# Kernel tuning notes

Measured on AMD Instinct MI355X. Metric: run time of the kernel, lower is better.

Reference implementation:

```python
import jax, jax.numpy as jnp
import numpy as np

B, CIN, P = 256, 128, 27
DIM, NCLS, COUT = 512, 16, 128
FC1_IN = 128 * 5 * 5  # conv stack on 27x27: 25->12->10->5


def conv2d(x, w, b):
    # x: [B,C,H,W], w: [O,I,kh,kw] (torch OIHW layout), VALID padding, stride 1
    y = jax.lax.conv_general_dilated(x, w, (1, 1), 'VALID',
                                     dimension_numbers=('NCHW', 'OIHW', 'NCHW'))
    return y + b[None, :, None, None]


def maxpool2(x):
    return jax.lax.reduce_window(x, -jnp.inf, jax.lax.max,
                                 (1, 1, 2, 2), (1, 1, 2, 2), 'VALID')


def essa(x, w_qkv, b_qkv, w_ln, b_ln):
    Bs, C, H, W = x.shape
    N = H * W
    t = x.reshape(Bs, C, N).transpose(0, 2, 1)          # [B,N,C]
    qkv = t @ w_qkv + b_qkv                              # [B,N,3C]
    q, k, v = jnp.split(qkv, 3, axis=-1)
    q = q - q.mean(-1, keepdims=True)
    k = k - k.mean(-1, keepdims=True)
    q2 = q * q
    k2 = k * k
    q2 = q2 / (q2.sum(-1, keepdims=True) + 1e-7)
    k2 = k2 / (k2.sum(-1, keepdims=True) + 1e-7)
    # F.normalize: L2-normalize q2 over channel dim, k2 over token dim
    q2 = q2 / jnp.maximum(jnp.linalg.norm(q2, axis=-1, keepdims=True), 1e-12)
    k2 = k2 / jnp.maximum(jnp.linalg.norm(k2, axis=-2, keepdims=True), 1e-12)
    kv = jnp.einsum('bnc,bnd->bcd', k2, v)               # [B,C,C]
    t2 = jnp.einsum('bnc,bcd->bnd', q2, kv) / float(np.sqrt(N))
    attn = (v + t2) @ w_ln + b_ln                        # [B,N,C]
    return attn.transpose(0, 2, 1).reshape(Bs, C, H, W)


def setup_inputs() -> dict:
    key = jax.random.key(0)
    ks = jax.random.split(key, 20)
    s = 0.02
    d = {
        'x': jax.random.normal(ks[0], (B, CIN, P, P), jnp.float32),
        'w_qkv': jax.random.normal(ks[1], (CIN, 3 * CIN), jnp.float32) * s,
        'b_qkv': jnp.zeros((3 * CIN,), jnp.float32),
        'w_ln': jax.random.normal(ks[2], (CIN, CIN), jnp.float32) * s,
        'b_ln': jnp.zeros((CIN,), jnp.float32),
        'w_ffn1': jax.random.normal(ks[3], (64, 2 * CIN, 1, 1), jnp.float32) * s,
        'b_ffn1': jnp.zeros((64,), jnp.float32),
        'w_ffn2': jax.random.normal(ks[4], (CIN, 64, 1, 1), jnp.float32) * s,
        'b_ffn2': jnp.zeros((CIN,), jnp.float32),
        'w_c1': jax.random.normal(ks[5], (64, CIN, 3, 3), jnp.float32) * s,
        'b_c1': jnp.zeros((64,), jnp.float32),
        'w_c2': jax.random.normal(ks[6], (128, 64, 3, 3), jnp.float32) * s,
        'b_c2': jnp.zeros((128,), jnp.float32),
        'w_fc1': jax.random.normal(ks[7], (FC1_IN, DIM), jnp.float32) * s,
        'b_fc1': jnp.zeros((DIM,), jnp.float32),
        'w_fc2': jax.random.normal(ks[8], (DIM, DIM), jnp.float32) * s,
        'b_fc2': jnp.zeros((DIM,), jnp.float32),
        'w_cls': jax.random.normal(ks[9], (DIM, NCLS), jnp.float32) * s,
        'b_cls': jnp.zeros((NCLS,), jnp.float32),
    }
    return d


def reference(x, w_qkv, b_qkv, w_ln, b_ln, w_ffn1, b_ffn1, w_ffn2, b_ffn2,
              w_c1, b_c1, w_c2, b_c2, w_fc1, b_fc1, w_fc2, b_fc2, w_cls, b_cls):
    x_essa = essa(x, w_qkv, b_qkv, w_ln, b_ln)
    cat = jnp.concatenate([x, x_essa], axis=1)           # [B,2C,H,W]
    h = jax.nn.leaky_relu(conv2d(cat, w_ffn1, b_ffn1))   # slope 0.01 = torch default
    x_en = conv2d(h, w_ffn2, b_ffn2) + x
    o1 = maxpool2(jax.nn.relu(conv2d(x_en, w_c1, b_c1)))
    o2 = maxpool2(jax.nn.relu(conv2d(o1, w_c2, b_c2)))
    o2 = o2.reshape(o2.shape[0], -1)                     # [B,3200]
    o3 = jax.nn.relu(o2 @ w_fc1 + b_fc1)
    o4 = jax.nn.relu(o3 @ w_fc2 + b_fc2)
    return o4 @ w_cls + b_cls                            # [B,num_classes]
```

## Files before the change

### kernel.cpp

```cpp
#include <hip/hip_runtime.h>
#include <hip/hip_bf16.h>

#define HB 256
#define HC 128
#define HN 729
#define NP 732
#define NT2 736

typedef __attribute__((ext_vector_type(8))) short bf16x8;
typedef __attribute__((ext_vector_type(4))) float f32x4;
typedef __attribute__((ext_vector_type(4))) unsigned int uint4v;
typedef unsigned short u16;

#define MFMA16(a,b,c) __builtin_amdgcn_mfma_f32_16x16x32_bf16((a),(b),(c),0,0,0)

__device__ __forceinline__ float wsum(float v) {
    #pragma unroll
    for (int m = 32; m >= 1; m >>= 1) v += __shfl_xor(v, m, 64);
    return v;
}
__device__ __forceinline__ u16 f2b(float f) {
    __hip_bfloat16 h = __float2bfloat16(f);
    return *reinterpret_cast<u16*>(&h);
}
__device__ __forceinline__ float b2f(u16 u) {
    __hip_bfloat16 h;
    *reinterpret_cast<u16*>(&h) = u;
    return __bfloat162float(h);
}
__device__ __forceinline__ unsigned int pk2(u16 a, u16 b) {
    return (unsigned int)a | ((unsigned int)b << 16);
}

__device__ __forceinline__ void stage_tile(char* lds, const u16* src, long srcK,
                                           int row0, int rowLim, int k0, int kLim,
                                           int R, int tid)
{
    for (int t = tid; t < R*8; t += 256) {
        int r = t >> 3, s = t & 7;
        uint4v val = {0u,0u,0u,0u};
        int gr = row0 + r;
        if (gr < rowLim && (k0 + s*8) < kLim)
            val = *(const uint4v*)(src + (long)gr*srcK + k0 + s*8);
        *(uint4v*)(lds + r*128 + ((s ^ (r & 7)) << 4)) = val;
    }
}
__device__ __forceinline__ bf16x8 frag_ld(const char* lds, int rbase, int k0, int lane)
{
    int r = rbase + (lane & 15);
    int s = (k0 >> 3) + (lane >> 4);
    return *(const bf16x8*)(lds + r*128 + ((s ^ (r & 7)) << 4));
}

__global__ void k_prep(const float* __restrict__ wf1, const float* __restrict__ wf2,
                       const float* __restrict__ wc1, const float* __restrict__ wc2,
                       const float* __restrict__ wqkv, const float* __restrict__ wln,
                       float* __restrict__ w1t, float* __restrict__ w2t,
                       u16* __restrict__ wqkvT, u16* __restrict__ wlnT,
                       u16* __restrict__ w1b, u16* __restrict__ w2b)
{
    int idx = blockIdx.x*256 + threadIdx.x;
    if (idx < 73728) {
        int row = idx >> 6, oc = idx & 63;
        int ic = row/9, tap = row - ic*9;
        w1t[idx] = wc1[(oc*128 + ic)*9 + tap];
    } else if (idx < 147456) {
        int t = idx - 73728; int row = t >> 7, oc = t & 127;
        int ic = row/9, tap = row - ic*9;
        w2t[t] = wc2[(oc*64 + ic)*9 + tap];
    } else if (idx < 196608) {
        int t = idx - 147456; int o = t >> 7, k = t & 127;
        wqkvT[t] = f2b(wqkv[k*384 + o]);
    } else if (idx < 212992) {
        int t = idx - 196608; int o = t >> 7, k = t & 127;
        wlnT[t] = f2b(wln[k*128 + o]);
    } else if (idx < 229376) {
        int t = idx - 212992;
        w1b[t] = f2b(wf1[t]);
    } else if (idx < 237568) {
        int t = idx - 229376;
        w2b[t] = f2b(wf2[t]);
    }
}

__global__ __launch_bounds__(256) void k_xbt(const float* __restrict__ x, u16* __restrict__ xbt)
{
    __shared__ float T[64*129];
    const int b = blockIdx.y, n0 = blockIdx.x*64, tid = threadIdx.x;
    for (int idx = tid; idx < 128*64; idx += 256) {
        int c = idx >> 6, j = idx & 63;
        int n = n0 + j;
        T[j*129 + c] = (n < HN) ? x[(size_t)(b*128 + c)*HN + n] : 0.f;
    }
    __syncthreads();
    for (int idx = tid; idx < 64*16; idx += 256) {
        int m = idx >> 4, cs = idx & 15;
        int n = n0 + m;
        if (n < HN) {
            const float* p = &T[m*129 + cs*8];
            uint4v V = { pk2(f2b(p[0]), f2b(p[1])), pk2(f2b(p[2]), f2b(p[3])),
                         pk2(f2b(p[4]), f2b(p[5])), pk2(f2b(p[6]), f2b(p[7])) };
            *(uint4v*)(xbt + ((long)b*HN + n)*128 + cs*8) = V;
        }
    }
}

__global__ __launch_bounds__(256) void k_gqkv(
    const u16* __restrict__ xbt, const u16* __restrict__ wqkvT, const float* __restrict__ bqkv,
    u16* __restrict__ qb, u16* __restrict__ kb, u16* __restrict__ vbt)
{
    __shared__ __align__(16) char smem[8192 + 49152];
    char* As = smem;
    char* Bs = smem + 8192;
    const int b = blockIdx.y, n0 = blockIdx.x*64, tid = threadIdx.x;
    const int lane = tid & 63, w = tid >> 6;
    f32x4 acc[4][6];
    #pragma unroll
    for (int i = 0; i < 4; ++i)
        #pragma unroll
        for (int j = 0; j < 6; ++j) acc[i][j] = (f32x4){0.f,0.f,0.f,0.f};
    const u16* Ab = xbt + (long)b*HN*128;
    for (int kt = 0; kt < 128; kt += 64) {
        stage_tile(As, Ab, 128, n0, HN, kt, 128, 64, tid);
        stage_tile(Bs, wqkvT, 128, 0, 384, kt, 128, 384, tid);
        __syncthreads();
        #pragma unroll
        for (int k0 = 0; k0 < 64; k0 += 32) {
            bf16x8 bf[6];
            #pragma unroll
            for (int j = 0; j < 6; ++j) bf[j] = frag_ld(Bs, (w*6 + j)*16, k0, lane);
            #pragma unroll
            for (int m = 0; m < 4; ++m) {
                bf16x8 af = frag_ld(As, m*16, k0, lane);
                #pragma unroll
                for (int j = 0; j < 6; ++j) acc[m][j] = MFMA16(af, bf[j], acc[m][j]);
            }
        }
        __syncthreads();
    }
    u16* E = (u16*)Bs;
    #pragma unroll
    for (int m = 0; m < 4; ++m)
        #pragma unroll
        for (int j = 0; j < 6; ++j) {
            int col = w*96 + j*16 + (lane & 15);
            float bia = bqkv[col];
            #pragma unroll
            for (int i = 0; i < 4; ++i) {
                int row = m*16 + (lane >> 4)*4 + i;
                E[row*384 + col] = f2b(acc[m][j][i] + bia);
            }
        }
    __syncthreads();
    for (int t = tid; t < 64*48; t += 256) {
        int r = t / 48, cs = t - r*48;
        int n = n0 + r;
        if (n < HN) {
            int col = cs*8;
            u16* dst = (col < 128) ? qb : (col < 256) ? kb : vbt;
            *(uint4v*)(dst + ((long)b*HN + n)*128 + (col & 127)) = *(const uint4v*)(E + r*384 + col);
        }
    }
}

__global__ __launch_bounds__(256) void k_postq(u16* __restrict__ qb)
{
    const int b = blockIdx.y;
    const int n = blockIdx.x*4 + (threadIdx.x >> 6);
    const int lane = threadIdx.x & 63;
    if (n >= HN) return;
    u16* p = qb + ((long)b*HN + n)*128;
    unsigned int u = *(const unsigned int*)(p + 2*lane);
    float f0 = b2f((u16)(u & 0xffff));
    float f1 = b2f((u16)(u >> 16));
    float m = wsum(f0 + f1) * (1.f/128.f);
    float a0 = f0 - m, a1 = f1 - m;
    float s0 = a0*a0, s1 = a1*a1;
    float S  = wsum(s0 + s1);
    float s4 = wsum(s0*s0 + s1*s1);
    float invS = 1.f / (S + 1e-7f);
    float nrm = sqrtf(s4) * invS;
    float sc = invS / fmaxf(nrm, 1e-12f);
    *(unsigned int*)(p + 2*lane) = pk2(f2b(s0*sc), f2b(s1*sc));
}

__global__ __launch_bounds__(256) void k_postk(const u16* __restrict__ kb, u16* __restrict__ k2t)
{
    __shared__ u16 KT[64*130];
    const int b = blockIdx.y, n0 = blockIdx.x*64, tid = threadIdx.x;
    const int lane = tid & 63, w = tid >> 6;
    for (int it = 0; it < 16; ++it) {
        int r = w*16 + it;
        int n = n0 + r;
        float f0 = 0.f, f1 = 0.f;
        if (n < HN) {
            unsigned int u = *(const unsigned int*)(kb + ((long)b*HN + n)*128 + 2*lane);
            f0 = b2f((u16)(u & 0xffff));
            f1 = b2f((u16)(u >> 16));
        }
        float m = wsum(f0 + f1) * (1.f/128.f);
        float a0 = f0 - m, a1 = f1 - m;
        float s0 = a0*a0, s1 = a1*a1;
        float S = wsum(s0 + s1);
        float invS = 1.f/(S + 1e-7f);
        *(unsigned int*)&KT[r*130 + 2*lane] = pk2(f2b(s0*invS), f2b(s1*invS));
    }
    __syncthreads();
    #pragma unroll
    for (int pass = 0; pass < 4; ++pass) {
        int c = pass*32 + (tid >> 3), j8 = tid & 7;
        u16 v[8];
        #pragma unroll
        for (int j = 0; j < 8; ++j) {
            int r = j8*8 + j;
            v[j] = (n0 + r < HN) ? KT[r*130 + c] : (u16)0;
        }
        int n = n0 + j8*8;
        if (n < NT2) {
            uint4v V = { pk2(v[0],v[1]), pk2(v[2],v[3]), pk2(v[4],v[5]), pk2(v[6],v[7]) };
            *(uint4v*)(k2t + ((long)b*128 + c)*NT2 + n) = V;
        }
    }
}

__global__ __launch_bounds__(256) void k_vT(const u16* __restrict__ vbt, u16* __restrict__ vtt)
{
    __shared__ u16 T[64*130];
    const int b = blockIdx.y, n0 = blockIdx.x*64, tid = threadIdx.x;
    for (int t = tid; t < 64*16; t += 256) {
        int r = t >> 4, cs = t & 15;
        int n = n0 + r;
        uint4v val = {0u,0u,0u,0u};
        if (n < HN) val = *(const uint4v*)(vbt + ((long)b*HN + n)*128 + cs*8);
        #pragma unroll
        for (int e = 0; e < 4; ++e)
            *(unsigned int*)&T[r*130 + cs*8 + e*2] = val[e];
    }
    __syncthreads();
    #pragma unroll
    for (int pass = 0; pass < 4; ++pass) {
        int d = pass*32 + (tid >> 3), j8 = tid & 7;
        u16 v[8];
        #pragma unroll
        for (int j = 0; j < 8; ++j) {
            int r = j8*8 + j;
            v[j] = (n0 + r < HN) ? T[r*130 + d] : (u16)0;
        }
        int n = n0 + j8*8;
        if (n < NT2) {
            uint4v V = { pk2(v[0],v[1]), pk2(v[2],v[3]), pk2(v[4],v[5]), pk2(v[6],v[7]) };
            *(uint4v*)(vtt + ((long)b*128 + d)*NT2 + n) = V;
        }
    }
}

__global__ __launch_bounds__(256) void k_coln(const u16* __restrict__ k2t, float* __restrict__ cn)
{
    long row = (long)blockIdx.x*4 + (threadIdx.x >> 6);
    int lane = threadIdx.x & 63;
    const u16* p = k2t + row*NT2;
    float s = 0.f;
    for (int i = lane; i < NT2/2; i += 64) {
        unsigned int u = *(const unsigned int*)(p + 2*i);
        float f0 = b2f((u16)(u & 0xffff));
        float f1 = b2f((u16)(u >> 16));
        s += f0*f0 + f1*f1;
    }
    s = wsum(s);
    if (lane == 0) cn[row] = 1.f / fmaxf(sqrtf(s), 1e-12f);
}

__global__ __launch_bounds__(256) void k_gkv(
    const u16* __restrict__ vtt, const u16* __restrict__ k2t,
    const float* __restrict__ cn, u16* __restrict__ kvT)
{
    __shared__ __align__(16) char smem[8192 + 16384 + 512];
    char* As = smem;
    char* Bs = smem + 8192;
    float* CNs = (float*)(smem + 8192 + 16384);
    const int b = blockIdx.y, d0 = blockIdx.x*64, tid = threadIdx.x;
    const int lane = tid & 63, w = tid >> 6;
    if (tid < 128) CNs[tid] = cn[b*128 + tid];
    f32x4 acc[4][2];
    #pragma unroll
    for (int i = 0; i < 4; ++i) { acc[i][0] = (f32x4){0,0,0,0}; acc[i][1] = (f32x4){0,0,0,0}; }
    const u16* Ab = vtt + (long)b*128*NT2;
    const u16* Bb = k2t + (long)b*128*NT2;
    for (int kt = 0; kt < NT2; kt += 64) {
        stage_tile(As, Ab, NT2, d0, 128, kt, NT2, 64, tid);
        stage_tile(Bs, Bb, NT2, 0, 128, kt, NT2, 128, tid);
        __syncthreads();
        #pragma unroll
        for (int k0 = 0; k0 < 64; k0 += 32) {
            bf16x8 bf[2];
            bf[0] = frag_ld(Bs, (w*2 + 0)*16, k0, lane);
            bf[1] = frag_ld(Bs, (w*2 + 1)*16, k0, lane);
            #pragma unroll
            for (int m = 0; m < 4; ++m) {
                bf16x8 af = frag_ld(As, m*16, k0, lane);
                acc[m][0] = MFMA16(af, bf[0], acc[m][0]);
                acc[m][1] = MFMA16(af, bf[1], acc[m][1]);
            }
        }
        __syncthreads();
    }
    u16* E = (u16*)Bs;
    #pragma unroll
    for (int m = 0; m < 4; ++m)
        #pragma unroll
        for (int j = 0; j < 2; ++j) {
            int col = w*32 + j*16 + (lane & 15);
            float s = CNs[col];
            #pragma unroll
            for (int i = 0; i < 4; ++i) {
                int row = m*16 + (lane >> 4)*4 + i;
                E[row*128 + col] = f2b(acc[m][j][i] * s);
            }
        }
    __syncthreads();
    for (int t = tid; t < 64*16; t += 256) {
        int r = t >> 4, cs = t & 15;
        *(uint4v*)(kvT + ((long)b*128 + d0 + r)*128 + cs*8) = *(const uint4v*)(E + r*128 + cs*8);
    }
}

__global__ __launch_bounds__(256) void k_gt2u(
    const u16* __restrict__ q2b, const u16* __restrict__ kvT,
    const u16* __restrict__ vbt, u16* __restrict__ ubt)
{
    __shared__ __align__(16) char smem[8192 + 16384];
    char* As = smem;
    char* Bs = smem + 8192;
    const int b = blockIdx.y, n0 = blockIdx.x*64, tid = threadIdx.x;
    const int lane = tid & 63, w = tid >> 6;
    f32x4 acc[4][2];
    #pragma unroll
    for (int i = 0; i < 4; ++i) { acc[i][0] = (f32x4){0,0,0,0}; acc[i][1] = (f32x4){0,0,0,0}; }
    const u16* Ab = q2b + (long)b*HN*128;
    const u16* Bb = kvT + (long)b*128*128;
    for (int kt = 0; kt < 128; kt += 64) {
        stage_tile(As, Ab, 128, n0, HN, kt, 128, 64, tid);
        stage_tile(Bs, Bb, 128, 0, 128, kt, 128, 128, tid);
        __syncthreads();
        #pragma unroll
        for (int k0 = 0; k0 < 64; k0 += 32) {
            bf16x8 bf[2];
            bf[0] = frag_ld(Bs, (w*2 + 0)*16, k0, lane);
            bf[1] = frag_ld(Bs, (w*2 + 1)*16, k0, lane);
            #pragma unroll
            for (int m = 0; m < 4; ++m) {
                bf16x8 af = frag_ld(As, m*16, k0, lane);
                acc[m][0] = MFMA16(af, bf[0], acc[m][0]);
                acc[m][1] = MFMA16(af, bf[1], acc[m][1]);
            }
        }
        __syncthreads();
    }
    u16* E = (u16*)Bs;
    const float sc = 1.f/27.f;
    #pragma unroll
    for (int m = 0; m < 4; ++m)
        #pragma unroll
        for (int j = 0; j < 2; ++j) {
            int col = w*32 + j*16 + (lane & 15);
            #pragma unroll
            for (int i = 0; i < 4; ++i) {
                int row = m*16 + (lane >> 4)*4 + i;
                E[row*128 + col] = f2b(acc[m][j][i] * sc);
            }
        }
    __syncthreads();
    for (int t = tid; t < 64*16; t += 256) {
        int r = t >> 4, cs = t & 15;
        int n = n0 + r;
        if (n < HN) {
            const u16* ep = E + r*128 + cs*8;
            const u16* vp = vbt + ((long)b*HN + n)*128 + cs*8;
            unsigned int wds[4];
            #pragma unroll
            for (int e = 0; e < 4; ++e)
                wds[e] = pk2(f2b(b2f(ep[e*2]) + b2f(vp[e*2])),
                             f2b(b2f(ep[e*2+1]) + b2f(vp[e*2+1])));
            uint4v V = { wds[0], wds[1], wds[2], wds[3] };
            *(uint4v*)(ubt + ((long)b*HN + n)*128 + cs*8) = V;
        }
    }
}

__global__ __launch_bounds__(256) void k_gattn(
    const u16* __restrict__ ubt, const u16* __restrict__ wlnT, const float* __restrict__ bln,
    u16* __restrict__ attnb)
{
    __shared__ __align__(16) char smem[8192 + 16384 + 512];
    char* As = smem;
    char* Bs = smem + 8192;
    float* BIAS = (float*)(smem + 8192 + 16384);
    const int b = blockIdx.y, n0 = blockIdx.x*64, tid = threadIdx.x;
    const int lane = tid & 63, w = tid >> 6;
    if (tid < 128) BIAS[tid] = bln[tid];
    f32x4 acc[4][2];
    #pragma unroll
    for (int i = 0; i < 4; ++i) { acc[i][0] = (f32x4){0,0,0,0}; acc[i][1] = (f32x4){0,0,0,0}; }
    const u16* Ab = ubt + (long)b*HN*128;
    for (int kt = 0; kt < 128; kt += 64) {
        stage_tile(As, Ab, 128, n0, HN, kt, 128, 64, tid);
        stage_tile(Bs, wlnT, 128, 0, 128, kt, 128, 128, tid);
        __syncthreads();
        #pragma unroll
        for (int k0 = 0; k0 < 64; k0 += 32) {
            bf16x8 bf[2];
            bf[0] = frag_ld(Bs, (w*2 + 0)*16, k0, lane);
            bf[1] = frag_ld(Bs, (w*2 + 1)*16, k0, lane);
            #pragma unroll
            for (int m = 0; m < 4; ++m) {
                bf16x8 af = frag_ld(As, m*16, k0, lane);
                acc[m][0] = MFMA16(af, bf[0], acc[m][0]);
                acc[m][1] = MFMA16(af, bf[1], acc[m][1]);
            }
        }
        __syncthreads();
    }
    u16* E = (u16*)Bs;
    #pragma unroll
    for (int m = 0; m < 4; ++m)
        #pragma unroll
        for (int j = 0; j < 2; ++j) {
            int col = w*32 + j*16 + (lane & 15);
            float bia = BIAS[col];
            #pragma unroll
            for (int i = 0; i < 4; ++i) {
                int row = m*16 + (lane >> 4)*4 + i;
                E[row*128 + col] = f2b(acc[m][j][i] + bia);
            }
        }
    __syncthreads();
    for (int t = tid; t < 64*16; t += 256) {
        int r = t >> 4, cs = t & 15;
        int n = n0 + r;
        if (n < HN)
            *(uint4v*)(attnb + ((long)b*HN + n)*128 + cs*8) = *(const uint4v*)(E + r*128 + cs*8);
    }
}

__global__ __launch_bounds__(256) void k_gffn1(
    const u16* __restrict__ xbt, const u16* __restrict__ attnb,
    const u16* __restrict__ w1b, const float* __restrict__ b1,
    u16* __restrict__ hb)
{
    __shared__ __align__(16) char smem[8192 + 8192 + 256];
    char* As = smem;
    char* Bs = smem + 8192;
    float* BIAS = (float*)(smem + 16384);
    const int b = blockIdx.y, n0 = blockIdx.x*64, tid = threadIdx.x;
    const int lane = tid & 63, w = tid >> 6;
    if (tid < 64) BIAS[tid] = b1[tid];
    f32x4 acc[4];
    #pragma unroll
    for (int i = 0; i < 4; ++i) acc[i] = (f32x4){0,0,0,0};
    const u16* Ax = xbt + (long)b*HN*128;
    const u16* Aa = attnb + (long)b*HN*128;
    for (int kt = 0; kt < 256; kt += 64) {
        if (kt < 128) stage_tile(As, Ax, 128, n0, HN, kt, 128, 64, tid);
        else          stage_tile(As, Aa, 128, n0, HN, kt - 128, 128, 64, tid);
        stage_tile(Bs, w1b, 256, 0, 64, kt, 256, 64, tid);
        __syncthreads();
        #pragma unroll
        for (int k0 = 0; k0 < 64; k0 += 32) {
            bf16x8 bf = frag_ld(Bs, w*16, k0, lane);
            #pragma unroll
            for (int m = 0; m < 4; ++m) {
                bf16x8 af = frag_ld(As, m*16, k0, lane);
                acc[m] = MFMA16(af, bf, acc[m]);
            }
        }
        __syncthreads();
    }
    u16* E = (u16*)Bs;
    #pragma unroll
    for (int m = 0; m < 4; ++m) {
        int col = w*16 + (lane & 15);
        float bia = BIAS[col];
        #pragma unroll
        for (int i = 0; i < 4; ++i) {
            int row = m*16 + (lane >> 4)*4 + i;
            float v = acc[m][i] + bia;
            E[row*64 + col] = f2b((v > 0.f) ? v : 0.01f*v);
        }
    }
    __syncthreads();
    for (int t = tid; t < 64*8; t += 256) {
        int r = t >> 3, cs = t & 7;
        int n = n0 + r;
        if (n < HN)
            *(uint4v*)(hb + ((long)b*HN + n)*64 + cs*8) = *(const uint4v*)(E + r*64 + cs*8);
    }
}

__global__ __launch_bounds__(256) void k_gffn2(
    const u16* __restrict__ hb, const u16* __restrict__ w2b, const float* __restrict__ b2,
    const float* __restrict__ x, float* __restrict__ xen)
{
    __shared__ __align__(16) char smem[8192 + 16384 + 512];
    char* As = smem;
    char* Bs = smem + 8192;
    float* BIAS = (float*)(smem + 8192 + 16384);
    const int b = blockIdx.y, n0 = blockIdx.x*64, tid = threadIdx.x;
    const int lane = tid & 63, w = tid >> 6;
    if (tid < 128) BIAS[tid] = b2[tid];
    f32x4 acc[4][2];
    #pragma unroll
    for (int i = 0; i < 4; ++i) { acc[i][0] = (f32x4){0,0,0,0}; acc[i][1] = (f32x4){0,0,0,0}; }
    const u16* Ab = hb + (long)b*HN*64;
    stage_tile(As, Ab, 64, n0, HN, 0, 64, 64, tid);
    stage_tile(Bs, w2b, 64, 0, 128, 0, 64, 128, tid);
    __syncthreads();
    #pragma unroll
    for (int k0 = 0; k0 < 64; k0 += 32) {
        bf16x8 bf[2];
        bf[0] = frag_ld(Bs, (w*2 + 0)*16, k0, lane);
        bf[1] = frag_ld(Bs, (w*2 + 1)*16, k0, lane);
        #pragma unroll
        for (int m = 0; m < 4; ++m) {
            bf16x8 af = frag_ld(As, m*16, k0, lane);
            acc[m][0] = MFMA16(af, bf[0], acc[m][0]);
            acc[m][1] = MFMA16(af, bf[1], acc[m][1]);
        }
    }
    __syncthreads();
    u16* E = (u16*)Bs;
    #pragma unroll
    for (int m = 0; m < 4; ++m)
        #pragma unroll
        for (int j = 0; j < 2; ++j) {
            int col = w*32 + j*16 + (lane & 15);
            float bia = BIAS[col];
            #pragma unroll
            for (int i = 0; i < 4; ++i) {
                int row = m*16 + (lane >> 4)*4 + i;
                E[row*128 + col] = f2b(acc[m][j][i] + bia);
            }
        }
    __syncthreads();
    #pragma unroll
    for (int pass = 0; pass < 16; ++pass) {
        int c = pass*8 + (tid >> 5), jj = tid & 31;
        int r = jj*2;
        int n = n0 + r;
        const float* xrow = x + ((long)b*128 + c)*HN;
        float* orow = xen + ((long)b*128 + c)*NP;
        if (n + 1 < HN) {
            float x0 = xrow[n], x1 = xrow[n+1];
            float2 ov;
            ov.x = b2f(E[r*128 + c]) + x0;
            ov.y = b2f(E[(r+1)*128 + c]) + x1;
            *(float2*)(orow + n) = ov;
        } else if (n < HN) {
            orow[n] = b2f(E[r*128 + c]) + xrow[n];
        }
    }
}

__global__ __launch_bounds__(256) void k_conv1(
    const float* __restrict__ xen, const float* __restrict__ w1t, const float* __restrict__ bias,
    float* __restrict__ pool1)
{
    __shared__ __align__(16) float XT[16*280];
    __shared__ __align__(16) float W[144*64];
    const int b = blockIdx.y;
    const int ty = blockIdx.x * 8;
    const int tid = threadIdx.x;
    const int row = tid & 7, og = tid >> 3;
    float acc[24][2] = {};
    for (int ic0 = 0; ic0 < 128; ic0 += 16) {
        __syncthreads();
        for (int idx = tid; idx < 4480; idx += 256) {
            int icc = idx / 280; int rem = idx - icc*280;
            int iy = rem / 28, ix = rem - iy*28;
            XT[idx] = (ix < 27) ? xen[((size_t)b*128 + ic0 + icc)*NP + (ty+iy)*27 + ix] : 0.f;
        }
        for (int idx = tid; idx < 9216; idx += 256) W[idx] = w1t[ic0*9*64 + idx];
        __syncthreads();
        for (int icc = 0; icc < 16; ++icc) {
            #pragma unroll
            for (int dy = 0; dy < 3; ++dy) {
                const float* ar = &XT[icc*280 + (row+dy)*28];
                float a[28];
                #pragma unroll
                for (int t = 0; t < 7; ++t) {
                    float4 f = *(const float4*)&ar[t*4];
                    a[t*4]=f.x; a[t*4+1]=f.y; a[t*4+2]=f.z; a[t*4+3]=f.w;
                }
                #pragma unroll
                for (int dx = 0; dx < 3; ++dx) {
                    float2 wv = *(const float2*)&W[(icc*9 + dy*3 + dx)*64 + og*2];
                    #pragma unroll
                    for (int px = 0; px < 24; ++px) {
                        acc[px][0] += a[px+dx]*wv.x;
                        acc[px][1] += a[px+dx]*wv.y;
                    }
                }
            }
        }
    }
    float b0 = bias[og*2], b1 = bias[og*2+1];
    float m[12][2];
    #pragma unroll
    for (int p = 0; p < 12; ++p) {
        float p00 = fmaxf(acc[2*p][0]+b0, 0.f), p10 = fmaxf(acc[2*p+1][0]+b0, 0.f);
        float p01 = fmaxf(acc[2*p][1]+b1, 0.f), p11 = fmaxf(acc[2*p+1][1]+b1, 0.f);
        m[p][0] = fmaxf(p00,p10); m[p][1] = fmaxf(p01,p11);
    }
    #pragma unroll
    for (int p = 0; p < 12; ++p) {
        m[p][0] = fmaxf(m[p][0], __shfl_xor(m[p][0], 1, 64));
        m[p][1] = fmaxf(m[p][1], __shfl_xor(m[p][1], 1, 64));
    }
    if ((row & 1) == 0) {
        int py = (ty + row) >> 1;
        #pragma unroll
        for (int p = 0; p < 12; ++p)
            *(float2*)&pool1[(((size_t)b*12 + py)*12 + p)*64 + og*2] = make_float2(m[p][0], m[p][1]);
    }
}

__global__ __launch_bounds__(256) void k_conv2(
    const float* __restrict__ pool1, const float* __restrict__ w2t, const float* __restrict__ bias,
    float* __restrict__ pool2)
{
    __shared__ __align__(16) float XT[8*144];
    __shared__ __align__(16) float W[72*32];
    const int b = blockIdx.y;
    const int oc0 = blockIdx.x * 32;
    const int tid = threadIdx.x;
    const int row = tid & 15, og = tid >> 4;
    float acc[10][2] = {};
    for (int ic0 = 0; ic0 < 64; ic0 += 8) {
        __syncthreads();
        for (int idx = tid; idx < 8*144; idx += 256) {
            int icc = idx & 7, pix = idx >> 3;
            XT[icc*144 + pix] = pool1[((size_t)b*144 + pix)*64 + ic0 + icc];
        }
        for (int idx = tid; idx < 72*32; idx += 256) {
            int r = idx >> 5, o = idx & 31;
            W[idx] = w2t[(ic0*9 + r)*128 + oc0 + o];
        }
        __syncthreads();
        if (row < 10) {
            for (int icc = 0; icc < 8; ++icc) {
                #pragma unroll
                for (int dy = 0; dy < 3; ++dy) {
                    const float* ar = &XT[icc*144 + (row+dy)*12];
                    float a[12];
                    #pragma unroll
                    for (int t = 0; t < 3; ++t) {
                        float4 f = *(const float4*)&ar[t*4];
                        a[t*4]=f.x; a[t*4+1]=f.y; a[t*4+2]=f.z; a[t*4+3]=f.w;
                    }
                    #pragma unroll
                    for (int dx = 0; dx < 3; ++dx) {
                        float2 wv = *(const float2*)&W[(icc*9 + dy*3 + dx)*32 + og*2];
                        #pragma unroll
                        for (int px = 0; px < 10; ++px) {
                            acc[px][0] += a[px+dx]*wv.x;
                            acc[px][1] += a[px+dx]*wv.y;
                        }
                    }
                }
            }
        }
    }
    float b0 = bias[oc0+og*2], b1 = bias[oc0+og*2+1];
    float m[5][2] = {};
    if (row < 10) {
        #pragma unroll
        for (int p = 0; p < 5; ++p) {
            float p00 = fmaxf(acc[2*p][0]+b0, 0.f), p10 = fmaxf(acc[2*p+1][0]+b0, 0.f);
            float p01 = fmaxf(acc[2*p][1]+b1, 0.f), p11 = fmaxf(acc[2*p+1][1]+b1, 0.f);
            m[p][0] = fmaxf(p00,p10); m[p][1] = fmaxf(p01,p11);
        }
    }
    #pragma unroll
    for (int p = 0; p < 5; ++p) {
        m[p][0] = fmaxf(m[p][0], __shfl_xor(m[p][0], 1, 64));
        m[p][1] = fmaxf(m[p][1], __shfl_xor(m[p][1], 1, 64));
    }
    if (row < 10 && (row & 1) == 0) {
        int py = row >> 1;
        #pragma unroll
        for (int p = 0; p < 5; ++p)
            *(float2*)&pool2[(((size_t)b*5 + py)*5 + p)*128 + oc0 + og*2] = make_float2(m[p][0], m[p][1]);
    }
}

__global__ void k_permute(const float* __restrict__ pool2, float* __restrict__ o2t)
{
    int k = blockIdx.x;
    int b = threadIdx.x;
    int c = k / 25, r = k - c*25;
    o2t[(size_t)k*256 + b] = pool2[((size_t)b*25 + r)*128 + c];
}

__global__ __launch_bounds__(256) void k_fc1(
    const float* __restrict__ o2t, const float* __restrict__ wfc1, float* __restrict__ part)
{
    __shared__ __align__(16) float A[64*64];
    __shared__ __align__(16) float W[64*64];
    const int m0 = blockIdx.x*64, nn0 = blockIdx.y*64, s = blockIdx.z;
    const int tid = threadIdx.x, tq = tid & 15, og = tid >> 4;
    float acc[4][4] = {};
    for (int chunk = s; chunk < 50; chunk += 4) {
        int k0 = chunk*64;
        __syncthreads();
        for (int idx = tid; idx < 4096; idx += 256) {
            int kk = idx >> 6, mm = idx & 63;
            A[idx] = o2t[(size_t)(k0+kk)*256 + m0 + mm];
        }
        for (int idx = tid; idx < 4096; idx += 256) {
            int kk = idx >> 6, nn = idx & 63;
            W[idx] = wfc1[(size_t)(k0+kk)*512 + nn0 + nn];
        }
        __syncthreads();
        for (int kk = 0; kk < 64; ++kk) {
            float4 a = *(const float4*)&A[kk*64 + tq*4];
            float4 wv = *(const float4*)&W[kk*64 + og*4];
            float av[4] = {a.x,a.y,a.z,a.w};
            float wl[4] = {wv.x,wv.y,wv.z,wv.w};
            #pragma unroll
            for (int i = 0; i < 4; ++i)
                #pragma unroll
                for (int jj = 0; jj < 4; ++jj) acc[i][jj] += av[i]*wl[jj];
        }
    }
    #pragma unroll
    for (int jn = 0; jn < 4; ++jn) {
        int n = nn0 + og*4 + jn;
        float4 o4 = make_float4(acc[0][jn], acc[1][jn], acc[2][jn], acc[3][jn]);
        *(float4*)&part[((size_t)s*512 + n)*256 + m0 + tq*4] = o4;
    }
}

__global__ void k_fc1red(const float* __restrict__ part, const float* __restrict__ bias,
                         float* __restrict__ o3t)
{
    int idx = blockIdx.x*256 + threadIdx.x;
    int n = idx >> 8, m = idx & 255;
    float vs = bias[n];
    #pragma unroll
    for (int s = 0; s < 4; ++s) vs += part[((size_t)s*512 + n)*256 + m];
    o3t[idx] = fmaxf(vs, 0.f);
}

__global__ __launch_bounds__(256) void k_fc2(
    const float* __restrict__ o3t, const float* __restrict__ wfc2, const float* __restrict__ bias,
    float* __restrict__ o4t)
{
    __shared__ __align__(16) float A[64*64];
    __shared__ __align__(16) float W[64*64];
    const int m0 = blockIdx.x*64, nn0 = blockIdx.y*64;
    const int tid = threadIdx.x, tq = tid & 15, og = tid >> 4;
    float acc[4][4] = {};
    for (int k0 = 0; k0 < 512; k0 += 64) {
        __syncthreads();
        for (int idx = tid; idx < 4096; idx += 256) {
            int kk = idx >> 6, mm = idx & 63;
            A[idx] = o3t[(size_t)(k0+kk)*256 + m0 + mm];
        }
        for (int idx = tid; idx < 4096; idx += 256) {
            int kk = idx >> 6, nn = idx & 63;
            W[idx] = wfc2[(size_t)(k0+kk)*512 + nn0 + nn];
        }
        __syncthreads();
        for (int kk = 0; kk < 64; ++kk) {
            float4 a = *(const float4*)&A[kk*64 + tq*4];
            float4 wv = *(const float4*)&W[kk*64 + og*4];
            float av[4] = {a.x,a.y,a.z,a.w};
            float wl[4] = {wv.x,wv.y,wv.z,wv.w};
            #pragma unroll
            for (int i = 0; i < 4; ++i)
                #pragma unroll
                for (int jj = 0; jj < 4; ++jj) acc[i][jj] += av[i]*wl[jj];
        }
    }
    #pragma unroll
    for (int jn = 0; jn < 4; ++jn) {
        int n = nn0 + og*4 + jn;
        float bb = bias[n];
        float4 o4 = make_float4(fmaxf(acc[0][jn]+bb,0.f), fmaxf(acc[1][jn]+bb,0.f),
                                fmaxf(acc[2][jn]+bb,0.f), fmaxf(acc[3][jn]+bb,0.f));
        *(float4*)&o4t[(size_t)n*256 + m0 + tq*4] = o4;
    }
}

__global__ __launch_bounds__(256) void k_cls(
    const float* __restrict__ o4t, const float* __restrict__ wcls, const float* __restrict__ bias,
    float* __restrict__ out)
{
    const int tid = threadIdx.x;
    const int ml = tid >> 4, nc = tid & 15;
    const int m = blockIdx.x*16 + ml;
    float acc = bias[nc];
    for (int k = 0; k < 512; ++k)
        acc += o4t[(size_t)k*256 + m] * wcls[k*16 + nc];
    out[m*16 + nc] = acc;
}

extern "C" void kernel_launch(void* const* d_in, const int* in_sizes, int n_in,
                              void* d_out, int out_size, void* d_ws, size_t ws_size,
                              hipStream_t stream)
{
    (void)in_sizes; (void)n_in; (void)out_size; (void)ws_size;
    const float* x    = (const float*)d_in[0];
    const float* wqkv = (const float*)d_in[1];
    const float* bqkv = (const float*)d_in[2];
    const float* wln  = (const float*)d_in[3];
    const float* bln  = (const float*)d_in[4];
    const float* wff1 = (const float*)d_in[5];
    const float* bff1 = (const float*)d_in[6];
    const float* wff2 = (const float*)d_in[7];
    const float* bff2 = (const float*)d_in[8];
    const float* wc1  = (const float*)d_in[9];
    const float* bc1  = (const float*)d_in[10];
    const float* wc2  = (const float*)d_in[11];
    const float* bc2  = (const float*)d_in[12];
    const float* wfc1 = (const float*)d_in[13];
    const float* bfc1 = (const float*)d_in[14];
    const float* wfc2 = (const float*)d_in[15];
    const float* bfc2 = (const float*)d_in[16];
    const float* wcls = (const float*)d_in[17];
    const float* bcls = (const float*)d_in[18];
    float* out = (float*)d_out;
    char* W = (char*)d_ws;

    u16*   ubt   = (u16*)(W + 0);
    u16*   xbt   = (u16*)(W + 47775744);
    float* xen   = (float*)(W + 0);
    u16*   qb    = (u16*)(W + 95944704);
    u16*   attnb = qb;
    float* pool2 = (float*)(W + 95944704);
    float* o2t   = (float*)(W + 95944704 + 4194304);
    float* part  = (float*)(W + 95944704 + 8388608);
    u16*   kb    = (u16*)(W + 143720448);
    u16*   vtt   = kb;
    u16*   hb    = kb;
    float* pool1 = (float*)(W + 143720448);
    u16*   vbt   = (u16*)(W + 191954944);
    float* o3t   = (float*)(W + 191954944);
    float* o4t   = (float*)(W + 191954944 + 1048576);
    u16*   k2t   = (u16*)(W + 239730688);
    u16*   kvT   = (u16*)(W + 287965184);
    float* cn    = (float*)(W + 296353792);
    float* w1t   = (float*)(W + 296353792 + 131072);
    float* w2t   = (float*)(W + 296353792 + 425984);
    u16*   wqkvT = (u16*)(W + 296353792 + 720896);
    u16*   wlnT  = (u16*)(W + 296353792 + 819200);
    u16*   w1b   = (u16*)(W + 296353792 + 851968);
    u16*   w2b   = (u16*)(W + 296353792 + 884736);

    k_prep<<<928, 256, 0, stream>>>(wff1, wff2, wc1, wc2, wqkv, wln,
                                    w1t, w2t, wqkvT, wlnT, w1b, w2b);
    k_xbt<<<dim3(12,256), 256, 0, stream>>>(x, xbt);
    k_gqkv<<<dim3(12,256), 256, 0, stream>>>(xbt, wqkvT, bqkv, qb, kb, vbt);
    k_postq<<<dim3(183,256), 256, 0, stream>>>(qb);
    k_postk<<<dim3(12,256), 256, 0, stream>>>(kb, k2t);
    k_vT<<<dim3(12,256), 256, 0, stream>>>(vbt, vtt);
    k_coln<<<8192, 256, 0, stream>>>(k2t, cn);
    k_gkv<<<dim3(2,256), 256, 0, stream>>>(vtt, k2t, cn, kvT);
    k_gt2u<<<dim3(12,256), 256, 0, stream>>>(qb, kvT, vbt, ubt);
    k_gattn<<<dim3(12,256), 256, 0, stream>>>(ubt, wlnT, bln, attnb);
    k_gffn1<<<dim3(12,256), 256, 0, stream>>>(xbt, attnb, w1b, bff1, hb);
    k_gffn2<<<dim3(12,256), 256, 0, stream>>>(hb, w2b, bff2, x, xen);
    k_conv1<<<dim3(3,256), 256, 0, stream>>>(xen, w1t, bc1, pool1);
    k_conv2<<<dim3(4,256), 256, 0, stream>>>(pool1, w2t, bc2, pool2);
    k_permute<<<3200, 256, 0, stream>>>(pool2, o2t);
    k_fc1<<<dim3(4,8,4), 256, 0, stream>>>(o2t, wfc1, part);
    k_fc1red<<<512, 256, 0, stream>>>(part, bfc1, o3t);
    k_fc2<<<dim3(4,8), 256, 0, stream>>>(o3t, wfc2, bfc2, o4t);
    k_cls<<<16, 256, 0, stream>>>(o4t, wcls, bcls, out);
}
```

Measured before the change: 1.126 ms.

## Run conv1 as bf16 MFMA implicit GEMM on token-major xen

The conv1 stage is rewritten as an implicit GEMM on bf16 MFMA tiles. Each block covers an 8x8 output patch and accumulates over 9 taps times 128 input channels, then fuses bias, ReLU and 2x2 max-pooling. To feed it, gffn2 now writes the residual output as token-major bf16 instead of channel-major fp32, staging x through LDS so the writes are vectorised. This replaces the scalar fp32 FMA conv and halves the intermediate traffic, at the cost of bf16 rounding on xen and weights and more LDS use in gffn2.

```diff
diff --git a/kernel.cpp b/kernel.cpp
--- a/kernel.cpp
+++ b/kernel.cpp
@@ -4,7 +4,6 @@
 #define HB 256
 #define HC 128
 #define HN 729
-#define NP 732
 #define NT2 736
 
 typedef __attribute__((ext_vector_type(8))) short bf16x8;
@@ -55,15 +54,15 @@
 __global__ void k_prep(const float* __restrict__ wf1, const float* __restrict__ wf2,
                        const float* __restrict__ wc1, const float* __restrict__ wc2,
                        const float* __restrict__ wqkv, const float* __restrict__ wln,
-                       float* __restrict__ w1t, float* __restrict__ w2t,
+                       u16* __restrict__ w1bT, float* __restrict__ w2t,
                        u16* __restrict__ wqkvT, u16* __restrict__ wlnT,
                        u16* __restrict__ w1b, u16* __restrict__ w2b)
 {
     int idx = blockIdx.x*256 + threadIdx.x;
     if (idx < 73728) {
-        int row = idx >> 6, oc = idx & 63;
-        int ic = row/9, tap = row - ic*9;
-        w1t[idx] = wc1[(oc*128 + ic)*9 + tap];
+        int o = idx / 1152, k = idx - o*1152;
+        int tap = k >> 7, ic = k & 127;
+        w1bT[idx] = f2b(wc1[(o*128 + ic)*9 + tap]);
     } else if (idx < 147456) {
         int t = idx - 73728; int row = t >> 7, oc = t & 127;
         int ic = row/9, tap = row - ic*9;
@@ -498,15 +497,21 @@
 
 __global__ __launch_bounds__(256) void k_gffn2(
     const u16* __restrict__ hb, const u16* __restrict__ w2b, const float* __restrict__ b2,
-    const float* __restrict__ x, float* __restrict__ xen)
+    const float* __restrict__ x, u16* __restrict__ xenb)
 {
     __shared__ __align__(16) char smem[8192 + 16384 + 512];
+    __shared__ __align__(16) float XT[128*65];
     char* As = smem;
     char* Bs = smem + 8192;
     float* BIAS = (float*)(smem + 8192 + 16384);
     const int b = blockIdx.y, n0 = blockIdx.x*64, tid = threadIdx.x;
     const int lane = tid & 63, w = tid >> 6;
     if (tid < 128) BIAS[tid] = b2[tid];
+    for (int idx = tid; idx < 8192; idx += 256) {
+        int c = idx >> 6, j = idx & 63;
+        int n = n0 + j;
+        XT[c*65 + j] = (n < HN) ? x[((long)b*128 + c)*HN + n] : 0.f;
+    }
     f32x4 acc[4][2];
     #pragma unroll
     for (int i = 0; i < 4; ++i) { acc[i][0] = (f32x4){0,0,0,0}; acc[i][1] = (f32x4){0,0,0,0}; }
@@ -541,85 +546,87 @@
             }
         }
     __syncthreads();
-    #pragma unroll
-    for (int pass = 0; pass < 16; ++pass) {
-        int c = pass*8 + (tid >> 5), jj = tid & 31;
-        int r = jj*2;
+    for (int t = tid; t < 64*16; t += 256) {
+        int r = t >> 4, cs = t & 15;
         int n = n0 + r;
-        const float* xrow = x + ((long)b*128 + c)*HN;
-        float* orow = xen + ((long)b*128 + c)*NP;
-        if (n + 1 < HN) {
-            float x0 = xrow[n], x1 = xrow[n+1];
-            float2 ov;
-            ov.x = b2f(E[r*128 + c]) + x0;
-            ov.y = b2f(E[(r+1)*128 + c]) + x1;
-            *(float2*)(orow + n) = ov;
-        } else if (n < HN) {
-            orow[n] = b2f(E[r*128 + c]) + xrow[n];
-        }
-    }
-}
-
-__global__ __launch_bounds__(256) void k_conv1(
-    const float* __restrict__ xen, const float* __restrict__ w1t, const float* __restrict__ bias,
+        if (n < HN) {
+            unsigned int wds[4];
+            #pragma unroll
+            for (int e = 0; e < 4; ++e) {
+                int c0 = cs*8 + e*2;
+                float v0 = b2f(E[r*128 + c0])     + XT[c0*65 + r];
+                float v1 = b2f(E[r*128 + c0 + 1]) + XT[(c0+1)*65 + r];
+                wds[e] = pk2(f2b(v0), f2b(v1));
+            }
+            uint4v V = { wds[0], wds[1], wds[2], wds[3] };
+            *(uint4v*)(xenb + ((long)b*HN + n)*128 + cs*8) = V;
+        }
+    }
+}
+
+__global__ __launch_bounds__(256) void k_gconv1(
+    const u16* __restrict__ xenb, const u16* __restrict__ w1bT, const float* __restrict__ bias,
     float* __restrict__ pool1)
 {
-    __shared__ __align__(16) float XT[16*280];
-    __shared__ __align__(16) float W[144*64];
+    __shared__ __align__(16) char smem[64*65*4];
+    char* As = smem;
+    char* Bs = smem + 8192;
     const int b = blockIdx.y;
-    const int ty = blockIdx.x * 8;
+    const int patch = blockIdx.x;
+    const int py0 = (patch / 3) * 8, px0 = (patch % 3) * 8;
     const int tid = threadIdx.x;
-    const int row = tid & 7, og = tid >> 3;
-    float acc[24][2] = {};
-    for (int ic0 = 0; ic0 < 128; ic0 += 16) {
-        __syncthreads();
-        for (int idx = tid; idx < 4480; idx += 256) {
-            int icc = idx / 280; int rem = idx - icc*280;
-            int iy = rem / 28, ix = rem - iy*28;
-            XT[idx] = (ix < 27) ? xen[((size_t)b*128 + ic0 + icc)*NP + (ty+iy)*27 + ix] : 0.f;
-        }
-        for (int idx = tid; idx < 9216; idx += 256) W[idx] = w1t[ic0*9*64 + idx];
-        __syncthreads();
-        for (int icc = 0; icc < 16; ++icc) {
-            #pragma unroll
-            for (int dy = 0; dy < 3; ++dy) {
-                const float* ar = &XT[icc*280 + (row+dy)*28];
-                float a[28];
+    const int lane = tid & 63, w = tid >> 6;
+    const u16* Ximg = xenb + (long)b*HN*128;
+    f32x4 acc[4];
+    #pragma unroll
+    for (int i = 0; i < 4; ++i) acc[i] = (f32x4){0,0,0,0};
+    for (int tap = 0; tap < 9; ++tap) {
+        const int dy = tap / 3, dx = tap - dy*3;
+        #pragma unroll
+        for (int kt = 0; kt < 2; ++kt) {
+            for (int t = tid; t < 512; t += 256) {
+                int r = t >> 3, s = t & 7;
+                int tok = (py0 + (r >> 3) + dy)*27 + px0 + (r & 7) + dx;
+                uint4v val = *(const uint4v*)(Ximg + (long)tok*128 + kt*64 + s*8);
+                *(uint4v*)(As + r*128 + ((s ^ (r & 7)) << 4)) = val;
+            }
+            stage_tile(Bs, w1bT, 1152, 0, 64, tap*128 + kt*64, 1152, 64, tid);
+            __syncthreads();
+            #pragma unroll
+            for (int k0 = 0; k0 < 64; k0 += 32) {
+                bf16x8 bf = frag_ld(Bs, w*16, k0, lane);
                 #pragma unroll
-                for (int t = 0; t < 7; ++t) {
-                    float4 f = *(const float4*)&ar[t*4];
-                    a[t*4]=f.x; a[t*4+1]=f.y; a[t*4+2]=f.z; a[t*4+3]=f.w;
+                for (int m = 0; m < 4; ++m) {
+                    bf16x8 af = frag_ld(As, m*16, k0, lane);
+                    acc[m] = MFMA16(af, bf, acc[m]);
                 }
-                #pragma unroll
-                for (int dx = 0; dx < 3; ++dx) {
-                    float2 wv = *(const float2*)&W[(icc*9 + dy*3 + dx)*64 + og*2];
-                    #pragma unroll
-                    for (int px = 0; px < 24; ++px) {
-                        acc[px][0] += a[px+dx]*wv.x;
-                        acc[px][1] += a[px+dx]*wv.y;
-                    }
-                }
-            }
-        }
-    }
-    float b0 = bias[og*2], b1 = bias[og*2+1];
-    float m[12][2];
-    #pragma unroll
-    for (int p = 0; p < 12; ++p) {
-        float p00 = fmaxf(acc[2*p][0]+b0, 0.f), p10 = fmaxf(acc[2*p+1][0]+b0, 0.f);
-        float p01 = fmaxf(acc[2*p][1]+b1, 0.f), p11 = fmaxf(acc[2*p+1][1]+b1, 0.f);
-        m[p][0] = fmaxf(p00,p10); m[p][1] = fmaxf(p01,p11);
-    }
-    #pragma unroll
-    for (int p = 0; p < 12; ++p) {
-        m[p][0] = fmaxf(m[p][0], __shfl_xor(m[p][0], 1, 64));
-        m[p][1] = fmaxf(m[p][1], __shfl_xor(m[p][1], 1, 64));
-    }
-    if ((row & 1) == 0) {
-        int py = (ty + row) >> 1;
-        #pragma unroll
-        for (int p = 0; p < 12; ++p)
-            *(float2*)&pool1[(((size_t)b*12 + py)*12 + p)*64 + og*2] = make_float2(m[p][0], m[p][1]);
+            }
+            __syncthreads();
+        }
+    }
+    float* E = (float*)smem;
+    {
+        int col = w*16 + (lane & 15);
+        float bia = bias[col];
+        #pragma unroll
+        for (int m = 0; m < 4; ++m)
+            #pragma unroll
+            for (int i = 0; i < 4; ++i) {
+                int row = m*16 + (lane >> 4)*4 + i;
+                E[row*65 + col] = fmaxf(acc[m][i] + bia, 0.f);
+            }
+    }
+    __syncthreads();
+    #pragma unroll
+    for (int pass = 0; pass < 4; ++pass) {
+        int oc = tid & 63;
+        int pp = (tid >> 6) + pass*4;
+        int pr = pp >> 2, pc = pp & 3;
+        int r0 = (2*pr)*8 + 2*pc;
+        float v = fmaxf(fmaxf(E[r0*65 + oc], E[(r0+1)*65 + oc]),
+                        fmaxf(E[(r0+8)*65 + oc], E[(r0+9)*65 + oc]));
+        int py = (py0 >> 1) + pr, px = (px0 >> 1) + pc;
+        pool1[(((long)b*12 + py)*12 + px)*64 + oc] = v;
     }
 }
 
@@ -832,8 +839,8 @@
     char* W = (char*)d_ws;
 
     u16*   ubt   = (u16*)(W + 0);
+    u16*   xenb  = (u16*)(W + 0);
     u16*   xbt   = (u16*)(W + 47775744);
-    float* xen   = (float*)(W + 0);
     u16*   qb    = (u16*)(W + 95944704);
     u16*   attnb = qb;
     float* pool2 = (float*)(W + 95944704);
@@ -849,7 +856,7 @@
     u16*   k2t   = (u16*)(W + 239730688);
     u16*   kvT   = (u16*)(W + 287965184);
     float* cn    = (float*)(W + 296353792);
-    float* w1t   = (float*)(W + 296353792 + 131072);
+    u16*   w1bT  = (u16*)(W + 296353792 + 131072);
     float* w2t   = (float*)(W + 296353792 + 425984);
     u16*   wqkvT = (u16*)(W + 296353792 + 720896);
     u16*   wlnT  = (u16*)(W + 296353792 + 819200);
@@ -857,7 +864,7 @@
     u16*   w2b   = (u16*)(W + 296353792 + 884736);
 
     k_prep<<<928, 256, 0, stream>>>(wff1, wff2, wc1, wc2, wqkv, wln,
-                                    w1t, w2t, wqkvT, wlnT, w1b, w2b);
+                                    w1bT, w2t, wqkvT, wlnT, w1b, w2b);
     k_xbt<<<dim3(12,256), 256, 0, stream>>>(x, xbt);
     k_gqkv<<<dim3(12,256), 256, 0, stream>>>(xbt, wqkvT, bqkv, qb, kb, vbt);
     k_postq<<<dim3(183,256), 256, 0, stream>>>(qb);
@@ -868,8 +875,8 @@
     k_gt2u<<<dim3(12,256), 256, 0, stream>>>(qb, kvT, vbt, ubt);
     k_gattn<<<dim3(12,256), 256, 0, stream>>>(ubt, wlnT, bln, attnb);
     k_gffn1<<<dim3(12,256), 256, 0, stream>>>(xbt, attnb, w1b, bff1, hb);
-    k_gffn2<<<dim3(12,256), 256, 0, stream>>>(hb, w2b, bff2, x, xen);
-    k_conv1<<<dim3(3,256), 256, 0, stream>>>(xen, w1t, bc1, pool1);
+    k_gffn2<<<dim3(12,256), 256, 0, stream>>>(hb, w2b, bff2, x, xenb);
+    k_gconv1<<<dim3(9,256), 256, 0, stream>>>(xenb, w1bT, bc1, pool1);
     k_conv2<<<dim3(4,256), 256, 0, stream>>>(pool1, w2t, bc2, pool2);
     k_permute<<<3200, 256, 0, stream>>>(pool2, o2t);
     k_fc1<<<dim3(4,8,4), 256, 0, stream>>>(o2t, wfc1, part);
```

Measured after the change: 949.5 us. 1.19x faster.
